# Optimization experiments

Hardware: AMD Instinct MI355X
Metric: run time of the kernel (lower is better)

The kernel has to match this reference:

```python
import jax, jax.numpy as jnp
import numpy as np

HIDDEN = 1024
HEADS = 16
BATCH = 2
SEQ = 2048
# dropout_p = 0.1 but module evaluated in eval mode (training=False) -> identity


def setup_inputs() -> dict:
    key = jax.random.key(0)
    k1, k2, k3 = jax.random.split(key, 3)
    x = jax.random.normal(k1, (BATCH, SEQ, HIDDEN), dtype=jnp.float32)
    # unit-scaling Linear: weight ~ N(0,1) (reset_parameters uses nn.init.normal_)
    w_qkv = jax.random.normal(k2, (3 * HIDDEN, HIDDEN), dtype=jnp.float32)
    w_o = jax.random.normal(k3, (HIDDEN, HIDDEN), dtype=jnp.float32)
    return {"x": x, "w_qkv": w_qkv, "w_o": w_o}


def reference(x, w_qkv, w_o):
    b, s, hid = x.shape
    heads = HEADS
    d = hid // heads
    # unit-scaled linear (constraint='to_output_scale'): y = x @ W.T * fan_in**-0.5
    qkv = (x @ w_qkv.T) * (hid ** -0.5)            # [b, s, 3*hid]
    # einops 'b s (z h d) -> z b h s d'
    qkv = qkv.reshape(b, s, 3, heads, d)
    q = jnp.transpose(qkv[:, :, 0], (0, 2, 1, 3))   # [b, h, s, d]
    k = jnp.transpose(qkv[:, :, 1], (0, 2, 1, 3))
    v = jnp.transpose(qkv[:, :, 2], (0, 2, 1, 3))
    # unit-scaled matmul: scale = inner_dim**-0.5
    scores = jnp.einsum('bhqd,bhkd->bhqk', q, k) * (d ** -0.5)  # [b, h, s, s]
    # unit-scaled softmax: output_scale = n / sqrt(n - 1)
    attn = jax.nn.softmax(scores, axis=-1) * (s / np.sqrt(s - 1.0))
    # dropout inactive (eval mode)
    out = jnp.einsum('bhqk,bhkd->bhqd', attn, v) * (s ** -0.5)  # inner dim = s
    out = jnp.transpose(out, (0, 2, 1, 3)).reshape(b, s, hid)   # 'b h s d -> b s (h d)'
    return (out @ w_o.T) * (hid ** -0.5)
```

## Files before the change

kernel.cpp:

```cpp
#include <hip/hip_runtime.h>

typedef unsigned short u16;
typedef __bf16 bf16x8 __attribute__((ext_vector_type(8)));
typedef _Float16 f16x8 __attribute__((ext_vector_type(8)));
typedef float f32x4 __attribute__((ext_vector_type(4)));
typedef unsigned short u16x4 __attribute__((ext_vector_type(4)));

#define HID 1024
#define SEQ 2048
#define NH 16
#define DH 64

__device__ __forceinline__ u16 f2h(float f) {
  return __builtin_bit_cast(u16, (_Float16)f);
}
__device__ __forceinline__ f32x4 mfma_h(f16x8 a, f16x8 b, f32x4 c) {
  return __builtin_amdgcn_mfma_f32_16x16x32_f16(a, b, c, 0, 0, 0);
}
__device__ __forceinline__ void g2l16(const u16* g, u16* l) {
  __builtin_amdgcn_global_load_lds(
      (const __attribute__((address_space(1))) unsigned int*)g,
      (__attribute__((address_space(3))) unsigned int*)l, 16, 0, 0);
}

__global__ __launch_bounds__(256) void cvt16_kernel(
    const float* __restrict__ src, u16* __restrict__ dst, int n4) {
  int i = blockIdx.x * 256 + threadIdx.x;
  if (i >= n4) return;
  const float4 v = ((const float4*)src)[i];
  u16x4 o;
  o[0] = f2h(v.x); o[1] = f2h(v.y); o[2] = f2h(v.z); o[3] = f2h(v.w);
  *(u16x4*)&dst[i * 4] = o;
}

__global__ __launch_bounds__(256) void split16_kernel(
    const float* __restrict__ src, u16* __restrict__ hi, u16* __restrict__ lo, int n4) {
  int i = blockIdx.x * 256 + threadIdx.x;
  if (i >= n4) return;
  const float4 v = ((const float4*)src)[i];
  float vv[4] = {v.x, v.y, v.z, v.w};
  u16x4 h, l;
#pragma unroll
  for (int j = 0; j < 4; ++j) {
    _Float16 hh = (_Float16)vv[j];
    h[j] = __builtin_bit_cast(u16, hh);
    l[j] = f2h(vv[j] - (float)hh);
  }
  *(u16x4*)&hi[i * 4] = h;
  *(u16x4*)&lo[i * 4] = l;
}

__global__ __launch_bounds__(256, 3) void gemm_qkv(
    const u16* __restrict__ a16, const u16* __restrict__ b16,
    u16* __restrict__ qf, u16* __restrict__ kf, u16* __restrict__ vtf) {
  __shared__ __align__(16) u16 la[128 * 32], lb[128 * 32];
  const int t = threadIdx.x;
  const int lane = t & 63, w = t >> 6;
  const int wr = w >> 1, wc = w & 1;
  const int lr = lane & 15, lg = lane >> 4;
  const int br = blockIdx.x, bc = blockIdx.y;
  const f32x4 fzero = {0.f, 0.f, 0.f, 0.f};
  f32x4 acc[4][4];
#pragma unroll
  for (int i = 0; i < 4; ++i)
#pragma unroll
    for (int j = 0; j < 4; ++j) acc[i][j] = fzero;
  const int srow = t >> 2, scol = (t & 3) << 3;
  const u16* ga = a16 + (size_t)(br * 128 + srow) * HID + scol;
  const u16* gb = b16 + (size_t)(bc * 128 + srow) * HID + scol;
  const int lo16 = t * 8;
  for (int kk = 0; kk < HID; kk += 32) {
    g2l16(ga + kk, &la[lo16]);
    g2l16(ga + kk + (size_t)64 * HID, &la[lo16 + 2048]);
    g2l16(gb + kk, &lb[lo16]);
    g2l16(gb + kk + (size_t)64 * HID, &lb[lo16 + 2048]);
    __syncthreads();
    f16x8 ah[4], bh[4];
#pragma unroll
    for (int i = 0; i < 4; ++i)
      ah[i] = *(const f16x8*)&la[(wr * 64 + i * 16 + lr) * 32 + lg * 8];
#pragma unroll
    for (int j = 0; j < 4; ++j)
      bh[j] = *(const f16x8*)&lb[(wc * 64 + j * 16 + lr) * 32 + lg * 8];
#pragma unroll
    for (int i = 0; i < 4; ++i)
#pragma unroll
      for (int j = 0; j < 4; ++j) acc[i][j] = mfma_h(ah[i], bh[j], acc[i][j]);
    __syncthreads();
  }
  const int m0 = br * 128 + wr * 64, n0 = bc * 128 + wc * 64;
#pragma unroll
  for (int i = 0; i < 4; ++i)
#pragma unroll
    for (int j = 0; j < 4; ++j)
#pragma unroll
      for (int r = 0; r < 4; ++r) {
        int row = m0 + i * 16 + lg * 4 + r;
        int col = n0 + j * 16 + lr;
        float val = acc[i][j][r] * 0.03125f;
        int b = row >> 11, s = row & 2047;
        int z = col >> 10, hh = (col >> 6) & 15, d = col & 63;
        int bhid = b * NH + hh;
        if (z == 0) {
          qf[((size_t)bhid * SEQ + s) * DH + d] = f2h(val * 0.125f);
        } else if (z == 1) {
          kf[((size_t)bhid * SEQ + s) * DH + d] = f2h(val);
        } else {
          vtf[((size_t)bhid * DH + d) * SEQ + s] = f2h(val);
        }
      }
}

__global__ __launch_bounds__(256, 2) void gemm_proj(
    const u16* __restrict__ a16,
    const u16* __restrict__ b_hi, const u16* __restrict__ b_lo,
    float* __restrict__ out) {
  __shared__ __align__(16) u16 la[128 * 32];
  __shared__ __align__(16) u16 lbh[64 * 32], lbl[64 * 32];
  const int t = threadIdx.x;
  const int lane = t & 63, w = t >> 6;
  const int wr = w >> 1, wc = w & 1;
  const int lr = lane & 15, lg = lane >> 4;
  const int br = blockIdx.x, bc = blockIdx.y;
  const f32x4 fzero = {0.f, 0.f, 0.f, 0.f};
  f32x4 acc[4][2];
#pragma unroll
  for (int i = 0; i < 4; ++i)
#pragma unroll
    for (int j = 0; j < 2; ++j) acc[i][j] = fzero;
  const int srow = t >> 2, scol = (t & 3) << 3;
  const u16* ga = a16 + (size_t)(br * 128 + srow) * HID + scol;
  const u16* gbh = b_hi + (size_t)(bc * 64 + srow) * HID + scol;
  const u16* gbl = b_lo + (size_t)(bc * 64 + srow) * HID + scol;
  const int lo16 = t * 8;
  for (int kk = 0; kk < HID; kk += 32) {
    g2l16(ga + kk, &la[lo16]);
    g2l16(ga + kk + (size_t)64 * HID, &la[lo16 + 2048]);
    g2l16(gbh + kk, &lbh[lo16]);
    g2l16(gbl + kk, &lbl[lo16]);
    __syncthreads();
    f16x8 ah[4], bh[2], bl[2];
#pragma unroll
    for (int i = 0; i < 4; ++i)
      ah[i] = *(const f16x8*)&la[(wr * 64 + i * 16 + lr) * 32 + lg * 8];
#pragma unroll
    for (int j = 0; j < 2; ++j) {
      int o = (wc * 32 + j * 16 + lr) * 32 + lg * 8;
      bh[j] = *(const f16x8*)&lbh[o];
      bl[j] = *(const f16x8*)&lbl[o];
    }
#pragma unroll
    for (int i = 0; i < 4; ++i)
#pragma unroll
      for (int j = 0; j < 2; ++j) {
        acc[i][j] = mfma_h(ah[i], bh[j], acc[i][j]);
        acc[i][j] = mfma_h(ah[i], bl[j], acc[i][j]);
      }
    __syncthreads();
  }
  const int m0 = br * 128 + wr * 64, n0 = bc * 64 + wc * 32;
#pragma unroll
  for (int i = 0; i < 4; ++i)
#pragma unroll
    for (int j = 0; j < 2; ++j)
#pragma unroll
      for (int r = 0; r < 4; ++r) {
        int row = m0 + i * 16 + lg * 4 + r;
        int col = n0 + j * 16 + lr;
        out[(size_t)row * HID + col] = acc[i][j][r] * 0.03125f;
      }
}

__global__ __launch_bounds__(256, 2) void attn_kernel(
    const u16* __restrict__ qf, const u16* __restrict__ kf,
    const u16* __restrict__ vtf, u16* __restrict__ o16) {
  __shared__ __align__(16) u16 lk[2][64 * 64];
  __shared__ __align__(16) u16 lv[2][64 * 64];
  __shared__ __align__(16) u16 lp[128 * 64];
  const int t = threadIdx.x;
  const int lane = t & 63, w = t >> 6;
  const int lr = lane & 15, lg = lane >> 4;
  const int bh = blockIdx.x, qt = blockIdx.y;
  const size_t base_qk = (size_t)bh * SEQ * DH;
  const size_t base_vt = (size_t)bh * DH * SEQ;

  f16x8 qfr[2][2];
#pragma unroll
  for (int rt = 0; rt < 2; ++rt)
#pragma unroll
    for (int ks = 0; ks < 2; ++ks)
      qfr[rt][ks] = *(const f16x8*)&qf[base_qk +
          (size_t)(qt * 128 + w * 32 + rt * 16 + lr) * DH + ks * 32 + lg * 8];

  const f32x4 fzero = {0.f, 0.f, 0.f, 0.f};
  f32x4 acc_o[2][4];
  float l_i[2][4];
#pragma unroll
  for (int rt = 0; rt < 2; ++rt)
#pragma unroll
    for (int r = 0; r < 4; ++r) l_i[rt][r] = 0.f;
#pragma unroll
  for (int rt = 0; rt < 2; ++rt)
#pragma unroll
    for (int ct = 0; ct < 4; ++ct) acc_o[rt][ct] = fzero;

  const int srow = t >> 3;
  const int c16s = (t & 7) ^ (srow & 7);
  const int scol = c16s * 8;
  const int lo16 = t * 8;

  const u16* gk0 = kf + base_qk + (size_t)srow * DH + scol;
  const u16* gv0 = vtf + base_vt + (size_t)srow * SEQ + scol;

#define STAGE(buf, j)                                             \
  {                                                               \
    const u16* gk = gk0 + (size_t)(j) * 64 * DH;                  \
    g2l16(gk, &lk[buf][lo16]);                                    \
    g2l16(gk + 32 * DH, &lk[buf][lo16 + 2048]);                   \
    const u16* gv = gv0 + (j) * 64;                               \
    g2l16(gv, &lv[buf][lo16]);                                    \
    g2l16(gv + (size_t)32 * SEQ, &lv[buf][lo16 + 2048]);          \
  }

  STAGE(0, 0)

  const int lrh = lr >> 3, lrl = lr & 7;

  for (int j = 0; j < SEQ / 64; ++j) {
    const int cur = j & 1;
    __syncthreads();

    f32x4 sa[2][4];
#pragma unroll
    for (int rt = 0; rt < 2; ++rt)
#pragma unroll
      for (int ct = 0; ct < 4; ++ct) sa[rt][ct] = fzero;
#pragma unroll
    for (int ks = 0; ks < 2; ++ks)
#pragma unroll
      for (int ct = 0; ct < 4; ++ct) {
        int row = ct * 16 + lr;
        f16x8 kfr = *(const f16x8*)&lk[cur][row * 64 + (((ks * 4 + lg) ^ (row & 7)) << 3)];
#pragma unroll
        for (int rt = 0; rt < 2; ++rt) sa[rt][ct] = mfma_h(qfr[rt][ks], kfr, sa[rt][ct]);
      }

#pragma unroll
    for (int rt = 0; rt < 2; ++rt)
#pragma unroll
      for (int r = 0; r < 4; ++r) {
        float p0 = __expf(sa[rt][0][r]);
        float p1 = __expf(sa[rt][1][r]);
        float p2 = __expf(sa[rt][2][r]);
        float p3 = __expf(sa[rt][3][r]);
        l_i[rt][r] += (p0 + p1) + (p2 + p3);
        int prow = w * 32 + rt * 16 + lg * 4 + r;
        int pb = prow * 64 + lrl;
        int x = prow & 7;
        lp[pb + (((0 + lrh) ^ x) << 3)] = f2h(p0);
        lp[pb + (((2 + lrh) ^ x) << 3)] = f2h(p1);
        lp[pb + (((4 + lrh) ^ x) << 3)] = f2h(p2);
        lp[pb + (((6 + lrh) ^ x) << 3)] = f2h(p3);
      }
    __syncthreads();

    if (j + 1 < SEQ / 64) STAGE(cur ^ 1, j + 1)

#pragma unroll
    for (int ks = 0; ks < 2; ++ks) {
      f16x8 pfr[2];
#pragma unroll
      for (int rt = 0; rt < 2; ++rt) {
        int prow = w * 32 + rt * 16 + lr;
        pfr[rt] = *(const f16x8*)&lp[prow * 64 + (((ks * 4 + lg) ^ (prow & 7)) << 3)];
      }
#pragma unroll
      for (int ct = 0; ct < 4; ++ct) {
        int vrow = ct * 16 + lr;
        f16x8 vfr = *(const f16x8*)&lv[cur][vrow * 64 + (((ks * 4 + lg) ^ (vrow & 7)) << 3)];
#pragma unroll
        for (int rt = 0; rt < 2; ++rt) acc_o[rt][ct] = mfma_h(pfr[rt], vfr, acc_o[rt][ct]);
      }
    }
  }

#pragma unroll
  for (int rt = 0; rt < 2; ++rt)
#pragma unroll
    for (int r = 0; r < 4; ++r) {
      float l = l_i[rt][r];
      l += __shfl_xor(l, 1, 16);
      l += __shfl_xor(l, 2, 16);
      l += __shfl_xor(l, 4, 16);
      l += __shfl_xor(l, 8, 16);
      l_i[rt][r] = l;
    }

  const int b = bh >> 4, hh = bh & 15;
  const float fact = 1.00024426f;
#pragma unroll
  for (int rt = 0; rt < 2; ++rt)
#pragma unroll
    for (int r = 0; r < 4; ++r) {
      float inv = fact / l_i[rt][r];
      int s = qt * 128 + w * 32 + rt * 16 + lg * 4 + r;
#pragma unroll
      for (int ct = 0; ct < 4; ++ct) {
        int d = ct * 16 + lr;
        float val = acc_o[rt][ct][r] * inv;
        o16[((size_t)(b * SEQ + s)) * HID + hh * DH + d] = f2h(val);
      }
    }
}

extern "C" void kernel_launch(void* const* d_in, const int* in_sizes, int n_in,
                              void* d_out, int out_size, void* d_ws, size_t ws_size,
                              hipStream_t stream) {
  const float* x = (const float*)d_in[0];
  const float* w_qkv = (const float*)d_in[1];
  const float* w_o = (const float*)d_in[2];
  u16* ws = (u16*)d_ws;
  const size_t XS = (size_t)4096 * 1024;
  const size_t WQ = (size_t)3072 * 1024;
  const size_t WO = (size_t)1024 * 1024;
  u16* x16  = ws;           u16* wq16 = x16 + XS;
  u16* wo_h = wq16 + WQ;    u16* wo_l = wo_h + WO;
  u16* q_f  = wo_l + WO;    u16* k_f  = q_f + XS;
  u16* vt_f = k_f + XS;     u16* o16  = vt_f + XS;

  cvt16_kernel<<<(int)(XS / 4 / 256), 256, 0, stream>>>(x, x16, (int)(XS / 4));
  cvt16_kernel<<<(int)(WQ / 4 / 256), 256, 0, stream>>>(w_qkv, wq16, (int)(WQ / 4));
  split16_kernel<<<(int)(WO / 4 / 256), 256, 0, stream>>>(w_o, wo_h, wo_l, (int)(WO / 4));
  gemm_qkv<<<dim3(32, 24), 256, 0, stream>>>(x16, wq16, q_f, k_f, vt_f);
  attn_kernel<<<dim3(32, 16), 256, 0, stream>>>(q_f, k_f, vt_f, o16);
  gemm_proj<<<dim3(32, 16), 256, 0, stream>>>(o16, wo_h, wo_l, (float*)d_out);
}
```

Before: 197.4 us.

## Fuse conversion kernels, widen GEMM K-tile to 64 with XOR swizzle, use exp2

```diff
diff --git a/kernel.cpp b/kernel.cpp
--- a/kernel.cpp
+++ b/kernel.cpp
@@ -1,7 +1,6 @@
 #include <hip/hip_runtime.h>
 
 typedef unsigned short u16;
-typedef __bf16 bf16x8 __attribute__((ext_vector_type(8)));
 typedef _Float16 f16x8 __attribute__((ext_vector_type(8)));
 typedef float f32x4 __attribute__((ext_vector_type(4)));
 typedef unsigned short u16x4 __attribute__((ext_vector_type(4)));
@@ -23,37 +22,46 @@
       (__attribute__((address_space(3))) unsigned int*)l, 16, 0, 0);
 }
 
-__global__ __launch_bounds__(256) void cvt16_kernel(
-    const float* __restrict__ src, u16* __restrict__ dst, int n4) {
+#define NX4 ((4096 * 1024) / 4)
+#define NQ4 ((3072 * 1024) / 4)
+#define NO4 ((1024 * 1024) / 4)
+__global__ __launch_bounds__(256) void prep_kernel(
+    const float* __restrict__ x, const float* __restrict__ wq,
+    const float* __restrict__ wo,
+    u16* __restrict__ x16, u16* __restrict__ wq16,
+    u16* __restrict__ wo_h, u16* __restrict__ wo_l) {
   int i = blockIdx.x * 256 + threadIdx.x;
-  if (i >= n4) return;
-  const float4 v = ((const float4*)src)[i];
-  u16x4 o;
-  o[0] = f2h(v.x); o[1] = f2h(v.y); o[2] = f2h(v.z); o[3] = f2h(v.w);
-  *(u16x4*)&dst[i * 4] = o;
-}
-
-__global__ __launch_bounds__(256) void split16_kernel(
-    const float* __restrict__ src, u16* __restrict__ hi, u16* __restrict__ lo, int n4) {
-  int i = blockIdx.x * 256 + threadIdx.x;
-  if (i >= n4) return;
-  const float4 v = ((const float4*)src)[i];
-  float vv[4] = {v.x, v.y, v.z, v.w};
-  u16x4 h, l;
-#pragma unroll
-  for (int j = 0; j < 4; ++j) {
-    _Float16 hh = (_Float16)vv[j];
-    h[j] = __builtin_bit_cast(u16, hh);
-    l[j] = f2h(vv[j] - (float)hh);
-  }
-  *(u16x4*)&hi[i * 4] = h;
-  *(u16x4*)&lo[i * 4] = l;
+  if (i < NX4) {
+    const float4 v = ((const float4*)x)[i];
+    u16x4 o;
+    o[0] = f2h(v.x); o[1] = f2h(v.y); o[2] = f2h(v.z); o[3] = f2h(v.w);
+    *(u16x4*)&x16[i * 4] = o;
+  } else if (i < NX4 + NQ4) {
+    int k = i - NX4;
+    const float4 v = ((const float4*)wq)[k];
+    u16x4 o;
+    o[0] = f2h(v.x); o[1] = f2h(v.y); o[2] = f2h(v.z); o[3] = f2h(v.w);
+    *(u16x4*)&wq16[k * 4] = o;
+  } else {
+    int k = i - NX4 - NQ4;
+    const float4 v = ((const float4*)wo)[k];
+    float vv[4] = {v.x, v.y, v.z, v.w};
+    u16x4 h, l;
+#pragma unroll
+    for (int j = 0; j < 4; ++j) {
+      _Float16 hh = (_Float16)vv[j];
+      h[j] = __builtin_bit_cast(u16, hh);
+      l[j] = f2h(vv[j] - (float)hh);
+    }
+    *(u16x4*)&wo_h[k * 4] = h;
+    *(u16x4*)&wo_l[k * 4] = l;
+  }
 }
 
 __global__ __launch_bounds__(256, 3) void gemm_qkv(
     const u16* __restrict__ a16, const u16* __restrict__ b16,
     u16* __restrict__ qf, u16* __restrict__ kf, u16* __restrict__ vtf) {
-  __shared__ __align__(16) u16 la[128 * 32], lb[128 * 32];
+  __shared__ __align__(16) u16 la[128 * 64], lb[128 * 64];
   const int t = threadIdx.x;
   const int lane = t & 63, w = t >> 6;
   const int wr = w >> 1, wc = w & 1;
@@ -65,27 +73,36 @@
   for (int i = 0; i < 4; ++i)
 #pragma unroll
     for (int j = 0; j < 4; ++j) acc[i][j] = fzero;
-  const int srow = t >> 2, scol = (t & 3) << 3;
+  const int srow = t >> 3;
+  const int scol = ((t & 7) ^ (srow & 7)) << 3;
   const u16* ga = a16 + (size_t)(br * 128 + srow) * HID + scol;
   const u16* gb = b16 + (size_t)(bc * 128 + srow) * HID + scol;
   const int lo16 = t * 8;
-  for (int kk = 0; kk < HID; kk += 32) {
-    g2l16(ga + kk, &la[lo16]);
-    g2l16(ga + kk + (size_t)64 * HID, &la[lo16 + 2048]);
-    g2l16(gb + kk, &lb[lo16]);
-    g2l16(gb + kk + (size_t)64 * HID, &lb[lo16 + 2048]);
-    __syncthreads();
-    f16x8 ah[4], bh[4];
-#pragma unroll
-    for (int i = 0; i < 4; ++i)
-      ah[i] = *(const f16x8*)&la[(wr * 64 + i * 16 + lr) * 32 + lg * 8];
-#pragma unroll
-    for (int j = 0; j < 4; ++j)
-      bh[j] = *(const f16x8*)&lb[(wc * 64 + j * 16 + lr) * 32 + lg * 8];
-#pragma unroll
-    for (int i = 0; i < 4; ++i)
-#pragma unroll
-      for (int j = 0; j < 4; ++j) acc[i][j] = mfma_h(ah[i], bh[j], acc[i][j]);
+  for (int kk = 0; kk < HID; kk += 64) {
+#pragma unroll
+    for (int p = 0; p < 4; ++p) {
+      g2l16(ga + kk + (size_t)(p * 32) * HID, &la[lo16 + p * 2048]);
+      g2l16(gb + kk + (size_t)(p * 32) * HID, &lb[lo16 + p * 2048]);
+    }
+    __syncthreads();
+#pragma unroll
+    for (int ks = 0; ks < 2; ++ks) {
+      f16x8 ah[4], bh[4];
+#pragma unroll
+      for (int i = 0; i < 4; ++i) {
+        int row = wr * 64 + i * 16 + lr;
+        ah[i] = *(const f16x8*)&la[row * 64 + (((ks * 4 + lg) ^ (row & 7)) << 3)];
+      }
+#pragma unroll
+      for (int j = 0; j < 4; ++j) {
+        int row = wc * 64 + j * 16 + lr;
+        bh[j] = *(const f16x8*)&lb[row * 64 + (((ks * 4 + lg) ^ (row & 7)) << 3)];
+      }
+#pragma unroll
+      for (int i = 0; i < 4; ++i)
+#pragma unroll
+        for (int j = 0; j < 4; ++j) acc[i][j] = mfma_h(ah[i], bh[j], acc[i][j]);
+    }
     __syncthreads();
   }
   const int m0 = br * 128 + wr * 64, n0 = bc * 128 + wc * 64;
@@ -102,7 +119,7 @@
         int z = col >> 10, hh = (col >> 6) & 15, d = col & 63;
         int bhid = b * NH + hh;
         if (z == 0) {
-          qf[((size_t)bhid * SEQ + s) * DH + d] = f2h(val * 0.125f);
+          qf[((size_t)bhid * SEQ + s) * DH + d] = f2h(val * 0.18033688f);
         } else if (z == 1) {
           kf[((size_t)bhid * SEQ + s) * DH + d] = f2h(val);
         } else {
@@ -115,8 +132,8 @@
     const u16* __restrict__ a16,
     const u16* __restrict__ b_hi, const u16* __restrict__ b_lo,
     float* __restrict__ out) {
-  __shared__ __align__(16) u16 la[128 * 32];
-  __shared__ __align__(16) u16 lbh[64 * 32], lbl[64 * 32];
+  __shared__ __align__(16) u16 la[128 * 64];
+  __shared__ __align__(16) u16 lbh[64 * 64], lbl[64 * 64];
   const int t = threadIdx.x;
   const int lane = t & 63, w = t >> 6;
   const int wr = w >> 1, wc = w & 1;
@@ -128,34 +145,45 @@
   for (int i = 0; i < 4; ++i)
 #pragma unroll
     for (int j = 0; j < 2; ++j) acc[i][j] = fzero;
-  const int srow = t >> 2, scol = (t & 3) << 3;
+  const int srow = t >> 3;
+  const int scol = ((t & 7) ^ (srow & 7)) << 3;
   const u16* ga = a16 + (size_t)(br * 128 + srow) * HID + scol;
   const u16* gbh = b_hi + (size_t)(bc * 64 + srow) * HID + scol;
   const u16* gbl = b_lo + (size_t)(bc * 64 + srow) * HID + scol;
   const int lo16 = t * 8;
-  for (int kk = 0; kk < HID; kk += 32) {
-    g2l16(ga + kk, &la[lo16]);
-    g2l16(ga + kk + (size_t)64 * HID, &la[lo16 + 2048]);
-    g2l16(gbh + kk, &lbh[lo16]);
-    g2l16(gbl + kk, &lbl[lo16]);
-    __syncthreads();
-    f16x8 ah[4], bh[2], bl[2];
-#pragma unroll
-    for (int i = 0; i < 4; ++i)
-      ah[i] = *(const f16x8*)&la[(wr * 64 + i * 16 + lr) * 32 + lg * 8];
-#pragma unroll
-    for (int j = 0; j < 2; ++j) {
-      int o = (wc * 32 + j * 16 + lr) * 32 + lg * 8;
-      bh[j] = *(const f16x8*)&lbh[o];
-      bl[j] = *(const f16x8*)&lbl[o];
-    }
-#pragma unroll
-    for (int i = 0; i < 4; ++i)
+  for (int kk = 0; kk < HID; kk += 64) {
+#pragma unroll
+    for (int p = 0; p < 4; ++p)
+      g2l16(ga + kk + (size_t)(p * 32) * HID, &la[lo16 + p * 2048]);
+#pragma unroll
+    for (int p = 0; p < 2; ++p) {
+      g2l16(gbh + kk + (size_t)(p * 32) * HID, &lbh[lo16 + p * 2048]);
+      g2l16(gbl + kk + (size_t)(p * 32) * HID, &lbl[lo16 + p * 2048]);
+    }
+    __syncthreads();
+#pragma unroll
+    for (int ks = 0; ks < 2; ++ks) {
+      f16x8 ah[4], bh[2], bl[2];
+#pragma unroll
+      for (int i = 0; i < 4; ++i) {
+        int row = wr * 64 + i * 16 + lr;
+        ah[i] = *(const f16x8*)&la[row * 64 + (((ks * 4 + lg) ^ (row & 7)) << 3)];
+      }
 #pragma unroll
       for (int j = 0; j < 2; ++j) {
-        acc[i][j] = mfma_h(ah[i], bh[j], acc[i][j]);
-        acc[i][j] = mfma_h(ah[i], bl[j], acc[i][j]);
-      }
+        int row = wc * 32 + j * 16 + lr;
+        int o = row * 64 + (((ks * 4 + lg) ^ (row & 7)) << 3);
+        bh[j] = *(const f16x8*)&lbh[o];
+        bl[j] = *(const f16x8*)&lbl[o];
+      }
+#pragma unroll
+      for (int i = 0; i < 4; ++i)
+#pragma unroll
+        for (int j = 0; j < 2; ++j) {
+          acc[i][j] = mfma_h(ah[i], bh[j], acc[i][j]);
+          acc[i][j] = mfma_h(ah[i], bl[j], acc[i][j]);
+        }
+    }
     __syncthreads();
   }
   const int m0 = br * 128 + wr * 64, n0 = bc * 64 + wc * 32;
@@ -205,8 +233,7 @@
     for (int ct = 0; ct < 4; ++ct) acc_o[rt][ct] = fzero;
 
   const int srow = t >> 3;
-  const int c16s = (t & 7) ^ (srow & 7);
-  const int scol = c16s * 8;
+  const int scol = ((t & 7) ^ (srow & 7)) << 3;
   const int lo16 = t * 8;
 
   const u16* gk0 = kf + base_qk + (size_t)srow * DH + scol;
@@ -249,10 +276,10 @@
     for (int rt = 0; rt < 2; ++rt)
 #pragma unroll
       for (int r = 0; r < 4; ++r) {
-        float p0 = __expf(sa[rt][0][r]);
-        float p1 = __expf(sa[rt][1][r]);
-        float p2 = __expf(sa[rt][2][r]);
-        float p3 = __expf(sa[rt][3][r]);
+        float p0 = exp2f(sa[rt][0][r]);
+        float p1 = exp2f(sa[rt][1][r]);
+        float p2 = exp2f(sa[rt][2][r]);
+        float p3 = exp2f(sa[rt][3][r]);
         l_i[rt][r] += (p0 + p1) + (p2 + p3);
         int prow = w * 32 + rt * 16 + lg * 4 + r;
         int pb = prow * 64 + lrl;
@@ -328,9 +355,8 @@
   u16* q_f  = wo_l + WO;    u16* k_f  = q_f + XS;
   u16* vt_f = k_f + XS;     u16* o16  = vt_f + XS;
 
-  cvt16_kernel<<<(int)(XS / 4 / 256), 256, 0, stream>>>(x, x16, (int)(XS / 4));
-  cvt16_kernel<<<(int)(WQ / 4 / 256), 256, 0, stream>>>(w_qkv, wq16, (int)(WQ / 4));
-  split16_kernel<<<(int)(WO / 4 / 256), 256, 0, stream>>>(w_o, wo_h, wo_l, (int)(WO / 4));
+  prep_kernel<<<(NX4 + NQ4 + NO4) / 256, 256, 0, stream>>>(
+      x, w_qkv, w_o, x16, wq16, wo_h, wo_l);
   gemm_qkv<<<dim3(32, 24), 256, 0, stream>>>(x16, wq16, q_f, k_f, vt_f);
   attn_kernel<<<dim3(32, 16), 256, 0, stream>>>(q_f, k_f, vt_f, o16);
   gemm_proj<<<dim3(32, 16), 256, 0, stream>>>(o16, wo_h, wo_l, (float*)d_out);
```

Result: slower. 207.7 us (+5.2%).
